# Kernel tuning notes

Measured on AMD Instinct MI355X. Metric: run time of the kernel, lower is better.

The kernel has to match this reference:

```python
import jax, jax.numpy as jnp
import numpy as np

B, KL, XL, DIM, H, PB = 4, 128, 4096, 256, 8, 8
HD = DIM // H
SCALE = HD ** -0.5
N_DIS = 64 + 2


def setup_inputs() -> dict:
    key = jax.random.key(0)
    ks = jax.random.split(key, 10)
    x = jax.random.normal(ks[0], (B, XL, DIM), jnp.float32)
    kernal = jax.random.normal(ks[1], (B, KL, DIM), jnp.float32)
    rd = jax.random.randint(ks[2], (B, KL, XL), 0, N_DIS)
    polar_pos = jax.random.randint(ks[3], (B, KL, XL), 0, PB)
    att_mask = jax.random.uniform(ks[4], (B, H, XL, KL)) < 0.1
    W_qkv = jax.random.normal(ks[5], (DIM, 3 * DIM), jnp.float32) * 0.02
    dis_embed = jax.random.normal(ks[6], (N_DIS, H), jnp.float32) * 0.02
    polar_emb = jax.random.normal(ks[7], (PB, 1), jnp.float32) * 0.02
    W_proj = jax.random.normal(ks[8], (DIM, DIM), jnp.float32) * 0.02
    b_proj = jnp.zeros((DIM,), jnp.float32)
    return dict(x=x, kernal=kernal, rd=rd, polar_pos=polar_pos, att_mask=att_mask,
                W_qkv=W_qkv, dis_embed=dis_embed, polar_emb=polar_emb,
                W_proj=W_proj, b_proj=b_proj)


def _heads(t, h):
    b, n, d = t.shape
    return t.reshape(b, n, h, d // h).transpose(0, 2, 1, 3)  # b h n hd


def reference(x, kernal, rd, polar_pos, att_mask, W_qkv, dis_embed, polar_emb, W_proj, b_proj):
    b, xl, dim = x.shape
    kl = kernal.shape[1]
    h = H
    scale = (dim // h) ** -0.5

    q, k, v = [_heads(t, h) for t in jnp.split(x @ W_qkv, 3, axis=-1)]        # b h xl hd
    k_q, k_k, k_v = [_heads(t, h) for t in jnp.split(kernal @ W_qkv, 3, axis=-1)]  # b h kl hd

    rd_e = dis_embed[rd].transpose(0, 3, 1, 2)  # (b,kl,xl,h) -> (b,h,kl,xl)

    # kernel -> x attention scores
    k_x_attn = jnp.einsum('bhkd,bhxd->bhkx', k_q, k) * scale  # b h kl xl

    # main orientation: one-hot-weighted |attn| reduced over x, argmax over polar bins
    pp = jnp.broadcast_to(polar_pos[:, None], (b, h, kl, xl))  # b h kl xl
    polar_hot = jax.nn.one_hot(pp, PB, dtype=k_x_attn.dtype)   # b h kl xl o
    ori_sum = jnp.einsum('bhkx,bhkxo->bhko', jnp.abs(k_x_attn), polar_hot)
    main_ori = jnp.argmax(ori_sum, axis=-1)                    # b h kl
    new_polar = pp - main_ori[..., None]
    new_polar = jnp.where(new_polar < 0, new_polar + PB, new_polar)
    polar_bias = polar_emb[new_polar, 0]                       # b h kl xl

    mask_k = att_mask.transpose(0, 1, 3, 2)                    # b h kl xl
    k_x_attn = jnp.where(mask_k, jnp.asarray(-1e6, k_x_attn.dtype), k_x_attn)
    attn_k = jax.nn.softmax(k_x_attn + rd_e + polar_bias, axis=-1)
    k_out = jnp.einsum('bhkx,bhxd->bhkd', attn_k, v)
    k_out = k_out.transpose(0, 2, 1, 3).reshape(b, kl, dim) @ W_proj + b_proj

    # x -> kernel attention scores
    x_k_attn = jnp.einsum('bhxd,bhkd->bhxk', q, k_k) * scale   # b h xl kl
    x_k_attn = jnp.where(att_mask, jnp.asarray(-1e9, x_k_attn.dtype), x_k_attn)
    x_k_attn = jax.nn.softmax(x_k_attn + rd_e.transpose(0, 1, 3, 2)
                              + polar_bias.transpose(0, 1, 3, 2), axis=-1)
    x_out = jnp.einsum('bhxk,bhkd->bhxd', x_k_attn, k_v)
    x_out = x_out.transpose(0, 2, 1, 3).reshape(b, xl, dim) @ W_proj + b_proj

    return (x_out, k_out)
```

## Files before the change

### kernel.cpp

```cpp
#include <hip/hip_runtime.h>
#include <hip/hip_bf16.h>

#define B_    4
#define KL_   128
#define XL_   4096
#define DIM_  256
#define H_    8
#define HD_   32
#define PB_   8
#define NDIS_ 66
#define TDIM_ 768
#define SCALE_ 0.17677669529663687f
#define NS_   4
#define XCH_  (XL_ / NS_)
#define NCH2_ 64
#define KC2_  16

typedef float v4f __attribute__((ext_vector_type(4)));
typedef short v8s __attribute__((ext_vector_type(8)));

__device__ __forceinline__ unsigned short f2bf(float f) {
    __hip_bfloat16 h = __float2bfloat16(f);
    return __builtin_bit_cast(unsigned short, h);
}
__device__ __forceinline__ float bf2f(unsigned short u) {
    return __bfloat162float(__builtin_bit_cast(__hip_bfloat16, u));
}
__device__ __forceinline__ void cvt_hilo(float v, unsigned short& hi, unsigned short& lo) {
    hi = f2bf(v);
    lo = f2bf(v - bf2f(hi));
}

__global__ __launch_bounds__(256) void pack_mask(const int* __restrict__ att_mask,
                                                 unsigned int* __restrict__ mbits) {
    size_t wid = (size_t)blockIdx.x * 256 + threadIdx.x;
    const int* src = &att_mask[wid * 32];
    unsigned bits = 0;
#pragma unroll
    for (int i = 0; i < 8; ++i) {
        int4 m4 = *(const int4*)&src[i * 4];
        bits |= (m4.x ? 1u : 0u) << (i * 4 + 0);
        bits |= (m4.y ? 1u : 0u) << (i * 4 + 1);
        bits |= (m4.z ? 1u : 0u) << (i * 4 + 2);
        bits |= (m4.w ? 1u : 0u) << (i * 4 + 3);
    }
    mbits[wid] = bits;
}

__global__ __launch_bounds__(256) void cvt_mat(const float* __restrict__ A,
                                               unsigned short* __restrict__ Ah,
                                               unsigned short* __restrict__ Al,
                                               size_t n4) {
    size_t i = ((size_t)blockIdx.x * 256 + threadIdx.x);
    if (i >= n4) return;
    float4 v = *(const float4*)&A[i * 4];
    ushort4 h, l;
    cvt_hilo(v.x, h.x, l.x);
    cvt_hilo(v.y, h.y, l.y);
    cvt_hilo(v.z, h.z, l.z);
    cvt_hilo(v.w, h.w, l.w);
    *(ushort4*)&Ah[i * 4] = h;
    *(ushort4*)&Al[i * 4] = l;
}

__global__ __launch_bounds__(256) void cvt_wT(const float* __restrict__ W,
                                              unsigned short* __restrict__ Wh,
                                              unsigned short* __restrict__ Wl,
                                              int K, int N) {
    int n = blockIdx.x, k = threadIdx.x;
    float v = W[(size_t)k * N + n];
    unsigned short h, l;
    cvt_hilo(v, h, l);
    Wh[(size_t)n * K + k] = h;
    Wl[(size_t)n * K + k] = l;
}

__global__ __launch_bounds__(256) void cvt_kq(const float* __restrict__ qkv_k,
                                              unsigned short* __restrict__ Kqh_g,
                                              unsigned short* __restrict__ Kql_g) {
    const int bh = blockIdx.x;
    const int b = bh >> 3, h = bh & 7;
    const int tid = threadIdx.x;
    const int k = tid >> 1, dg = (tid & 1) * 16;
    const float* src = &qkv_k[((size_t)(b * KL_ + k)) * TDIM_ + h * HD_ + dg];
    unsigned short hi[16], lo[16];
#pragma unroll
    for (int j4 = 0; j4 < 4; ++j4) {
        float4 v = *(const float4*)&src[j4 * 4];
        cvt_hilo(v.x, hi[j4 * 4 + 0], lo[j4 * 4 + 0]);
        cvt_hilo(v.y, hi[j4 * 4 + 1], lo[j4 * 4 + 1]);
        cvt_hilo(v.z, hi[j4 * 4 + 2], lo[j4 * 4 + 2]);
        cvt_hilo(v.w, hi[j4 * 4 + 3], lo[j4 * 4 + 3]);
    }
    unsigned short* dh = &Kqh_g[((size_t)bh * KL_ + k) * HD_ + dg];
    unsigned short* dl = &Kql_g[((size_t)bh * KL_ + k) * HD_ + dg];
    *(uint4*)&dh[0] = *(uint4*)&hi[0];
    *(uint4*)&dh[8] = *(uint4*)&hi[8];
    *(uint4*)&dl[0] = *(uint4*)&lo[0];
    *(uint4*)&dl[8] = *(uint4*)&lo[8];
}

__global__ __launch_bounds__(256) void gemm_mfma(const unsigned short* __restrict__ Ah,
                                                 const unsigned short* __restrict__ Al,
                                                 const unsigned short* __restrict__ Bh,
                                                 const unsigned short* __restrict__ Bl,
                                                 float* __restrict__ C,
                                                 const float* __restrict__ bias,
                                                 int M, int N, int K) {
    __shared__ __align__(16) unsigned short Ah_s[128][40];
    __shared__ __align__(16) unsigned short Al_s[128][40];
    __shared__ __align__(16) unsigned short Bh_s[128][40];
    __shared__ __align__(16) unsigned short Bl_s[128][40];
    const int tid = threadIdx.x;
    const int w = tid >> 6, lane = tid & 63;
    const int c = lane & 15, q = lane >> 4;
    const int bm = blockIdx.y * 128, bn = blockIdx.x * 128;
    const int srow = tid >> 1, shf = (tid & 1) * 16;

    v4f acc[2][8] = {};
    for (int k0 = 0; k0 < K; k0 += 32) {
        __syncthreads();
        {
            const size_t ab = (size_t)(bm + srow) * K + k0 + shf;
            *(uint4*)&Ah_s[srow][shf] = *(const uint4*)&Ah[ab];
            *(uint4*)&Ah_s[srow][shf + 8] = *(const uint4*)&Ah[ab + 8];
            *(uint4*)&Al_s[srow][shf] = *(const uint4*)&Al[ab];
            *(uint4*)&Al_s[srow][shf + 8] = *(const uint4*)&Al[ab + 8];
            const size_t bb = (size_t)(bn + srow) * K + k0 + shf;
            *(uint4*)&Bh_s[srow][shf] = *(const uint4*)&Bh[bb];
            *(uint4*)&Bh_s[srow][shf + 8] = *(const uint4*)&Bh[bb + 8];
            *(uint4*)&Bl_s[srow][shf] = *(const uint4*)&Bl[bb];
            *(uint4*)&Bl_s[srow][shf + 8] = *(const uint4*)&Bl[bb + 8];
        }
        __syncthreads();
        v8s afh[2], afl[2];
#pragma unroll
        for (int mt = 0; mt < 2; ++mt) {
            afh[mt] = *(v8s*)&Ah_s[w * 32 + mt * 16 + c][q * 8];
            afl[mt] = *(v8s*)&Al_s[w * 32 + mt * 16 + c][q * 8];
        }
#pragma unroll
        for (int nt = 0; nt < 8; ++nt) {
            v8s bfh = *(v8s*)&Bh_s[nt * 16 + c][q * 8];
            v8s bfl = *(v8s*)&Bl_s[nt * 16 + c][q * 8];
#pragma unroll
            for (int mt = 0; mt < 2; ++mt) {
                acc[mt][nt] = __builtin_amdgcn_mfma_f32_16x16x32_bf16(afl[mt], bfh, acc[mt][nt], 0, 0, 0);
                acc[mt][nt] = __builtin_amdgcn_mfma_f32_16x16x32_bf16(afh[mt], bfl, acc[mt][nt], 0, 0, 0);
                acc[mt][nt] = __builtin_amdgcn_mfma_f32_16x16x32_bf16(afh[mt], bfh, acc[mt][nt], 0, 0, 0);
            }
        }
    }
#pragma unroll
    for (int mt = 0; mt < 2; ++mt) {
#pragma unroll
        for (int nt = 0; nt < 8; ++nt) {
            int col = bn + nt * 16 + c;
            float bv = bias ? bias[col] : 0.0f;
#pragma unroll
            for (int r = 0; r < 4; ++r) {
                int row = bm + w * 32 + mt * 16 + q * 4 + r;
                C[(size_t)row * N + col] = acc[mt][nt][r] + bv;
            }
        }
    }
}

__global__ __launch_bounds__(256) void gemm64(const float* __restrict__ A,
                                              const float* __restrict__ Bw,
                                              float* __restrict__ C,
                                              const float* __restrict__ bias,
                                              int M, int N, int K) {
    __shared__ __align__(16) float As[16][68];
    __shared__ __align__(16) float Bs[16][64];
    const int tid = threadIdx.x;
    const int tx = tid & 15, ty = tid >> 4;
    const int bn = blockIdx.x * 64, bm = blockIdx.y * 64;
    const int am = tid >> 2, ac = tid & 3;
    float acc[4][4] = {};
    for (int k0 = 0; k0 < K; k0 += 16) {
        float4 a4 = *(const float4*)&A[(size_t)(bm + am) * K + k0 + ac * 4];
        As[ac * 4 + 0][am] = a4.x;
        As[ac * 4 + 1][am] = a4.y;
        As[ac * 4 + 2][am] = a4.z;
        As[ac * 4 + 3][am] = a4.w;
        *(float4*)&Bs[ty][tx * 4] = *(const float4*)&Bw[(size_t)(k0 + ty) * N + bn + tx * 4];
        __syncthreads();
#pragma unroll
        for (int kk = 0; kk < 16; ++kk) {
            float4 av = *(const float4*)&As[kk][ty * 4];
            float4 bv = *(const float4*)&Bs[kk][tx * 4];
            float a[4] = {av.x, av.y, av.z, av.w};
            float b[4] = {bv.x, bv.y, bv.z, bv.w};
#pragma unroll
            for (int i = 0; i < 4; ++i)
#pragma unroll
                for (int j = 0; j < 4; ++j) acc[i][j] += a[i] * b[j];
        }
        __syncthreads();
    }
#pragma unroll
    for (int i = 0; i < 4; ++i) {
        int m = bm + ty * 4 + i;
#pragma unroll
        for (int j = 0; j < 4; ++j) {
            int n = bn + tx * 4 + j;
            float v = acc[i][j];
            if (bias) v += bias[n];
            C[(size_t)m * N + n] = v;
        }
    }
}

__global__ __launch_bounds__(256) void score_bins_mfma4(const float* __restrict__ qkv_x,
                                                        const unsigned short* __restrict__ Kqh_g,
                                                        const unsigned short* __restrict__ Kql_g,
                                                        const int* __restrict__ rd,
                                                        const int* __restrict__ polar_pos,
                                                        const unsigned int* __restrict__ mbits,
                                                        const float* __restrict__ dis_embed,
                                                        __hip_bfloat16* __restrict__ Sg,
                                                        float* __restrict__ binspart) {
    const int b = blockIdx.z, h = blockIdx.y, xc = blockIdx.x;
    const int x0 = xc * 64;
    const int tid = threadIdx.x;
    const int w = tid >> 6, lane = tid & 63;
    const int c15 = lane & 15, q = lane >> 4;
    const size_t bh = (size_t)(b * H_ + h);

    __shared__ unsigned int mskb[64][5];
    __shared__ float de_h[NDIS_];
    __shared__ float binsL[8][4][16][PB_];
    __shared__ __align__(16) unsigned short Ss[2][16][72];

    {
        int xr = tid >> 2, kg = tid & 3;
        mskb[xr][kg] = mbits[(bh * XL_ + x0 + xr) * 4 + kg];
    }
    if (tid < NDIS_) de_h[tid] = dis_embed[tid * H_ + h];
    __syncthreads();

    v8s axh, axl;
    {
        const float* src = &qkv_x[((size_t)b * XL_ + x0 + w * 16 + c15) * TDIM_ + DIM_ + h * HD_ + q * 8];
        float4 v0 = *(const float4*)&src[0];
        float4 v1 = *(const float4*)&src[4];
        float vv[8] = {v0.x, v0.y, v0.z, v0.w, v1.x, v1.y, v1.z, v1.w};
#pragma unroll
        for (int j = 0; j < 8; ++j) {
            unsigned short hi, lo;
            cvt_hilo(vv[j], hi, lo);
            ((short*)&axh)[j] = (short)hi;
            ((short*)&axl)[j] = (short)lo;
        }
    }

    v8s bqh[2], bql[2];
    int4 r4[2], p4[2];
    auto load_nt = [&](int nt, int s) {
        const int k = nt * 16 + c15;
        const size_t kqoff = (bh * KL_ + k) * HD_ + q * 8;
        bqh[s] = *(const v8s*)&Kqh_g[kqoff];
        bql[s] = *(const v8s*)&Kql_g[kqoff];
        const size_t rowoff = ((size_t)(b * KL_ + k)) * XL_ + x0 + w * 16 + q * 4;
        r4[s] = *(const int4*)&rd[rowoff];
        p4[s] = *(const int4*)&polar_pos[rowoff];
    };
    load_nt(0, 0);

#pragma unroll
    for (int nt = 0; nt < 8; ++nt) {
        const int s = nt & 1;
        if (nt < 7) load_nt(nt + 1, s ^ 1);

        const int k = nt * 16 + c15;
        v4f D = {0.f, 0.f, 0.f, 0.f};
        D = __builtin_amdgcn_mfma_f32_16x16x32_bf16(axl, bqh[s], D, 0, 0, 0);
        D = __builtin_amdgcn_mfma_f32_16x16x32_bf16(axh, bql[s], D, 0, 0, 0);
        D = __builtin_amdgcn_mfma_f32_16x16x32_bf16(axh, bqh[s], D, 0, 0, 0);

        float bins[PB_] = {};
        {
            int rv[4] = {r4[s].x, r4[s].y, r4[s].z, r4[s].w};
            int pv[4] = {p4[s].x, p4[s].y, p4[s].z, p4[s].w};
            ushort4 pack;
#pragma unroll
            for (int r = 0; r < 4; ++r) {
                float sc = D[r] * SCALE_;
                float a = fabsf(sc);
                int pp = pv[r];
#pragma unroll
                for (int pb = 0; pb < PB_; ++pb) bins[pb] += (pp == pb) ? a : 0.0f;
                int xloc = w * 16 + q * 4 + r;
                int mbit = (mskb[xloc][k >> 5] >> (k & 31)) & 1;
                float sp = (mbit ? -1e6f : sc) + de_h[rv[r]];
                ((unsigned short*)&pack)[r] = f2bf(sp);
            }
            *(ushort4*)&Ss[s][c15][w * 16 + q * 4] = pack;
        }

#pragma unroll
        for (int pb = 0; pb < PB_; ++pb) {
            bins[pb] += __shfl_xor(bins[pb], 16);
            bins[pb] += __shfl_xor(bins[pb], 32);
        }
        if (q == 0) {
#pragma unroll
            for (int pb = 0; pb < PB_; ++pb) binsL[nt][w][c15][pb] = bins[pb];
        }

        __syncthreads();
        {
            int row = tid >> 4, seg = tid & 15;
            unsigned short* dst = (unsigned short*)Sg +
                (bh * KL_ + nt * 16 + row) * XL_ + x0 + seg * 4;
            *(uint2*)dst = *(const uint2*)&Ss[s][row][seg * 4];
        }
    }
    __syncthreads();
    {
        int k = tid >> 1, half = tid & 1;
        int nt = k >> 4, c = k & 15;
        float4 s = {0.f, 0.f, 0.f, 0.f};
#pragma unroll
        for (int w4 = 0; w4 < 4; ++w4) {
            float4 v = *(float4*)&binsL[nt][w4][c][half * 4];
            s.x += v.x; s.y += v.y; s.z += v.z; s.w += v.w;
        }
        *(float4*)&binspart[(bh * KL_ + k) * (NCH2_ * PB_) + xc * PB_ + half * 4] = s;
    }
}

__global__ __launch_bounds__(256) void bins_argmax(const float* __restrict__ binspart,
                                                   int* __restrict__ main_ori) {
    const int w = threadIdx.x >> 6, lane = threadIdx.x & 63;
    const int row = blockIdx.x * 4 + w;
    float s[PB_];
#pragma unroll
    for (int pb = 0; pb < PB_; ++pb) s[pb] = 0.0f;
    if (lane < NCH2_) {
        const float* bp = &binspart[(size_t)row * (NCH2_ * PB_) + lane * PB_];
#pragma unroll
        for (int pb = 0; pb < PB_; ++pb) s[pb] = bp[pb];
    }
#pragma unroll
    for (int m = 1; m < 64; m <<= 1)
#pragma unroll
        for (int pb = 0; pb < PB_; ++pb) s[pb] += __shfl_xor(s[pb], m);
    if (lane == 0) {
        float best = s[0];
        int bi = 0;
#pragma unroll
        for (int pb = 1; pb < PB_; ++pb)
            if (s[pb] > best) { best = s[pb]; bi = pb; }
        main_ori[row] = bi;
    }
}

__global__ __launch_bounds__(256) void flash_cached2(const float* __restrict__ qkv_x,
                                                     const __hip_bfloat16* __restrict__ Sg,
                                                     const int* __restrict__ polar_pos,
                                                     const float* __restrict__ polar_emb,
                                                     const int* __restrict__ main_ori,
                                                     float* __restrict__ part) {
    const int b = blockIdx.z, h = blockIdx.y;
    const int kch = blockIdx.x / NS_, xc = blockIdx.x % NS_;
    const int k0 = kch * KC2_;
    const int tid = threadIdx.x;
    const int ki = tid >> 4, xt = tid & 15;

    __shared__ __align__(16) float4 vs[64][9];
    __shared__ int pol_s[KC2_][68];
    __shared__ float pe[PB_];

    if (tid < PB_) pe[tid] = polar_emb[tid];
    const size_t xbase = (size_t)b * XL_;
    const size_t bh = (size_t)(b * H_ + h);
    const size_t row_k = bh * KL_ + k0 + ki;
    const int mo = main_ori[row_k];
    const int xbeg = xc * XCH_;

    float l = 0.f;
    float4 acc[8] = {};
    __syncthreads();
    for (int t = 0; t < XCH_ / 64; ++t) {
        const int x0 = xbeg + t * 64;
        __syncthreads();
#pragma unroll
        for (int i = 0; i < 2; ++i) {
            int id = tid + 256 * i;
            int row = id >> 3, c = id & 7;
            vs[row][c] = *(const float4*)&qkv_x[(xbase + x0 + row) * TDIM_ + 2 * DIM_ + h * HD_ + c * 4];
        }
        {
            int kk = tid >> 4, c = tid & 15;
            *(int4*)&pol_s[kk][c * 4] =
                *(const int4*)&polar_pos[(size_t)(b * KL_ + k0 + kk) * XL_ + x0 + c * 4];
        }
        __syncthreads();
#pragma unroll
        for (int j = 0; j < 4; ++j) {
            int xl = xt + 16 * j;
            int x = x0 + xl;
            float sp = __bfloat162float(Sg[row_k * XL_ + x]);
            int pp = pol_s[ki][xl];
            int np = pp - mo;
            np += (np >> 31) & PB_;
            float p = __expf(sp + pe[np]);
            l += p;
#pragma unroll
            for (int c = 0; c < 8; ++c) {
                float4 v = vs[xl][c];
                acc[c].x += p * v.x; acc[c].y += p * v.y;
                acc[c].z += p * v.z; acc[c].w += p * v.w;
            }
        }
    }
#pragma unroll
    for (int m = 1; m < 16; m <<= 1) {
        l += __shfl_xor(l, m, 16);
#pragma unroll
        for (int c = 0; c < 8; ++c) {
            acc[c].x += __shfl_xor(acc[c].x, m, 16);
            acc[c].y += __shfl_xor(acc[c].y, m, 16);
            acc[c].z += __shfl_xor(acc[c].z, m, 16);
            acc[c].w += __shfl_xor(acc[c].w, m, 16);
        }
    }
    if (xt == 0) {
        float* dst = &part[(size_t)(row_k * NS_ + xc) * 36];
#pragma unroll
        for (int c = 0; c < 8; ++c) *(float4*)&dst[c * 4] = acc[c];
        dst[32] = l;
    }
}

__global__ __launch_bounds__(256) void merge_cached(const float* __restrict__ part,
                                                    float* __restrict__ kout_pre) {
    const int tid = threadIdx.x;
    const int ri = tid >> 5, d = tid & 31;
    const int row = blockIdx.x * 8 + ri;
    float l = 0.f, a = 0.f;
#pragma unroll
    for (int c = 0; c < NS_; ++c) {
        const float* p = &part[(size_t)(row * NS_ + c) * 36];
        l += p[32];
        a += p[d];
    }
    int k = row & (KL_ - 1);
    int bh = row >> 7;
    int h = bh & (H_ - 1), b = bh >> 3;
    kout_pre[(size_t)(b * KL_ + k) * DIM_ + h * HD_ + d] = a / l;
}

__global__ __launch_bounds__(256) void attn_x_mfma(const float* __restrict__ qkv_x,
                                                   const float* __restrict__ qkv_k,
                                                   const int* __restrict__ rd,
                                                   const int* __restrict__ polar_pos,
                                                   const unsigned int* __restrict__ mbits,
                                                   const float* __restrict__ dis_embed,
                                                   const float* __restrict__ polar_emb,
                                                   const int* __restrict__ main_ori,
                                                   unsigned short* __restrict__ oh,
                                                   unsigned short* __restrict__ ol) {
    const int b = blockIdx.z, h = blockIdx.y;
    const int x0 = blockIdx.x * 64;
    const int tid = threadIdx.x;
    const int wave = tid >> 6, lane = tid & 63;
    const int c = lane & 15, q = lane >> 4;

    __shared__ __align__(16) unsigned short Kk_s[KL_][40];
    __shared__ __align__(16) unsigned short VT_s[HD_][136];
    __shared__ __align__(16) unsigned short P_s[4][16][136];
    __shared__ unsigned short rp_s[KL_][72];
    __shared__ unsigned int msk_s[64][5];
    __shared__ float de_h[NDIS_];
    __shared__ float pe[PB_];
    __shared__ int mo_s[KL_];

    const size_t bh = (size_t)(b * H_ + h);
    if (tid < NDIS_) de_h[tid] = dis_embed[tid * H_ + h];
    if (tid < PB_) pe[tid] = polar_emb[tid];
    if (tid < KL_) mo_s[tid] = main_ori[bh * KL_ + tid];

    {
        int row = tid >> 1, half = tid & 1;
        const float* src = &qkv_k[(size_t)(b * KL_ + row) * TDIM_ + h * HD_ + half * 16];
#pragma unroll
        for (int j = 0; j < 16; ++j) Kk_s[row][half * 16 + j] = f2bf(src[DIM_ + j]);
#pragma unroll
        for (int j = 0; j < 16; ++j) VT_s[half * 16 + j][row] = f2bf(src[2 * DIM_ + j]);
    }
    {
        int xr = tid >> 2, kg = tid & 3;
        msk_s[xr][kg] = mbits[(bh * XL_ + x0 + xr) * 4 + kg];
    }
    __syncthreads();

#pragma unroll
    for (int i = 0; i < 8; ++i) {
        int id = tid + 256 * i;
        int k = id >> 4, cc = id & 15;
        size_t gb = (size_t)(b * KL_ + k) * XL_ + x0 + cc * 4;
        int4 r4 = *(const int4*)&rd[gb];
        int4 p4 = *(const int4*)&polar_pos[gb];
        int mo = mo_s[k];
        int n0 = p4.x - mo; n0 += (n0 >> 31) & PB_;
        int n1 = p4.y - mo; n1 += (n1 >> 31) & PB_;
        int n2 = p4.z - mo; n2 += (n2 >> 31) & PB_;
        int n3 = p4.w - mo; n3 += (n3 >> 31) & PB_;
        rp_s[k][cc * 4 + 0] = (unsigned short)(r4.x | (n0 << 8));
        rp_s[k][cc * 4 + 1] = (unsigned short)(r4.y | (n1 << 8));
        rp_s[k][cc * 4 + 2] = (unsigned short)(r4.z | (n2 << 8));
        rp_s[k][cc * 4 + 3] = (unsigned short)(r4.w | (n3 << 8));
    }
    __syncthreads();

    v8s aq;
    {
        const float* qp = &qkv_x[(size_t)(b * XL_ + x0 + wave * 16 + c) * TDIM_ + h * HD_ + q * 8];
        float4 q0 = *(const float4*)&qp[0];
        float4 q1 = *(const float4*)&qp[4];
        aq[0] = (short)f2bf(q0.x); aq[1] = (short)f2bf(q0.y);
        aq[2] = (short)f2bf(q0.z); aq[3] = (short)f2bf(q0.w);
        aq[4] = (short)f2bf(q1.x); aq[5] = (short)f2bf(q1.y);
        aq[6] = (short)f2bf(q1.z); aq[7] = (short)f2bf(q1.w);
    }

    v4f S[8];
#pragma unroll
    for (int t = 0; t < 8; ++t) {
        v8s bk = *(v8s*)&Kk_s[t * 16 + c][q * 8];
        S[t] = __builtin_amdgcn_mfma_f32_16x16x32_bf16(aq, bk, (v4f){0.f, 0.f, 0.f, 0.f}, 0, 0, 0);
    }

    const int xloc = wave * 16;
    float lr[4] = {0.f, 0.f, 0.f, 0.f};
#pragma unroll
    for (int t = 0; t < 8; ++t) {
#pragma unroll
        for (int r = 0; r < 4; ++r) {
            int krow = t * 16 + c;
            int xrow = q * 4 + r;
            unsigned short rp = rp_s[krow][xloc + xrow];
            int mbit = (msk_s[xloc + xrow][krow >> 5] >> (krow & 31)) & 1;
            float sval = S[t][r] * SCALE_;
            float tval = (mbit ? -25.0f : sval) + de_h[rp & 0x7f] + pe[(rp >> 8) & 7];
            float p = __expf(tval);
            unsigned short pb = f2bf(p);
            P_s[wave][xrow][krow] = pb;
            lr[r] += bf2f(pb);
        }
    }
#pragma unroll
    for (int r = 0; r < 4; ++r) {
#pragma unroll
        for (int m = 1; m < 16; m <<= 1) lr[r] += __shfl_xor(lr[r], m);
    }
    __syncthreads();

    v4f O0 = {0.f, 0.f, 0.f, 0.f}, O1 = {0.f, 0.f, 0.f, 0.f};
#pragma unroll
    for (int kc = 0; kc < 4; ++kc) {
        v8s ap = *(v8s*)&P_s[wave][c][kc * 32 + q * 8];
        v8s bv0 = *(v8s*)&VT_s[c][kc * 32 + q * 8];
        v8s bv1 = *(v8s*)&VT_s[16 + c][kc * 32 + q * 8];
        O0 = __builtin_amdgcn_mfma_f32_16x16x32_bf16(ap, bv0, O0, 0, 0, 0);
        O1 = __builtin_amdgcn_mfma_f32_16x16x32_bf16(ap, bv1, O1, 0, 0, 0);
    }

#pragma unroll
    for (int r = 0; r < 4; ++r) {
        int xg = x0 + wave * 16 + q * 4 + r;
        float inv = 1.0f / lr[r];
        size_t obase = (size_t)(b * XL_ + xg) * DIM_ + h * HD_;
        float v0 = O0[r] * inv;
        float v1 = O1[r] * inv;
        unsigned short h0, l0, h1, l1;
        cvt_hilo(v0, h0, l0);
        cvt_hilo(v1, h1, l1);
        oh[obase + c] = h0;
        ol[obase + c] = l0;
        oh[obase + 16 + c] = h1;
        ol[obase + 16 + c] = l1;
    }
}

extern "C" void kernel_launch(void* const* d_in, const int* in_sizes, int n_in,
                              void* d_out, int out_size, void* d_ws, size_t ws_size,
                              hipStream_t stream) {
    const float* x         = (const float*)d_in[0];
    const float* kernal    = (const float*)d_in[1];
    const int* rd          = (const int*)d_in[2];
    const int* polar_pos   = (const int*)d_in[3];
    const int* att_mask    = (const int*)d_in[4];
    const float* W_qkv     = (const float*)d_in[5];
    const float* dis_embed = (const float*)d_in[6];
    const float* polar_emb = (const float*)d_in[7];
    const float* W_proj    = (const float*)d_in[8];
    const float* b_proj    = (const float*)d_in[9];
    float* out             = (float*)d_out;

    char* base = (char*)d_ws;
    size_t off = 0;
    auto alloc = [&](size_t bytes) { void* p = base + off; off = (off + bytes + 255) & ~255ULL; return p; };
    float* qkv_x    = (float*)alloc((size_t)B_ * XL_ * TDIM_ * 4);
    float* qkv_k    = (float*)alloc((size_t)B_ * KL_ * TDIM_ * 4);
    float* xout_pre = (float*)alloc((size_t)B_ * XL_ * DIM_ * 4);
    float* kout_pre = (float*)alloc((size_t)B_ * KL_ * DIM_ * 4);
    int* main_ori   = (int*)alloc(B_ * H_ * KL_ * 4);
    float* part     = (float*)alloc((size_t)B_ * H_ * KL_ * NS_ * 36 * 4);
    __hip_bfloat16* Sg = (__hip_bfloat16*)alloc((size_t)B_ * H_ * KL_ * XL_ * 2);
    unsigned short* wph = (unsigned short*)alloc((size_t)DIM_ * DIM_ * 2);
    unsigned short* wpl = (unsigned short*)alloc((size_t)DIM_ * DIM_ * 2);
    unsigned int* mbits = (unsigned int*)alloc((size_t)B_ * H_ * XL_ * (KL_ / 32) * 4);

    float* binspart = xout_pre;
    const size_t MX = (size_t)B_ * XL_;
    unsigned short* xh = (unsigned short*)Sg;
    unsigned short* xl_ = xh + MX * DIM_;
    unsigned short* wqh = (unsigned short*)part;
    unsigned short* wql = wqh + (size_t)TDIM_ * DIM_;
    unsigned short* kqh_g = wqh + 2 * (size_t)TDIM_ * DIM_;
    unsigned short* kql_g = kqh_g + (size_t)B_ * H_ * KL_ * HD_;
    unsigned short* oh = (unsigned short*)Sg;
    unsigned short* ol = oh + MX * DIM_;

    pack_mask<<<dim3((B_ * H_ * XL_ * (KL_ / 32)) / 256), 256, 0, stream>>>(att_mask, mbits);
    cvt_mat<<<dim3((MX * DIM_ / 4 + 255) / 256), 256, 0, stream>>>(x, xh, xl_, MX * DIM_ / 4);
    cvt_wT<<<dim3(TDIM_), DIM_, 0, stream>>>(W_qkv, wqh, wql, DIM_, TDIM_);
    cvt_wT<<<dim3(DIM_), DIM_, 0, stream>>>(W_proj, wph, wpl, DIM_, DIM_);

    gemm_mfma<<<dim3(TDIM_ / 128, MX / 128), 256, 0, stream>>>(
        xh, xl_, wqh, wql, qkv_x, nullptr, MX, TDIM_, DIM_);
    gemm64<<<dim3(TDIM_ / 64, (B_ * KL_) / 64), 256, 0, stream>>>(
        kernal, W_qkv, qkv_k, nullptr, B_ * KL_, TDIM_, DIM_);
    cvt_kq<<<dim3(B_ * H_), 256, 0, stream>>>(qkv_k, kqh_g, kql_g);

    score_bins_mfma4<<<dim3(NCH2_, H_, B_), 256, 0, stream>>>(
        qkv_x, kqh_g, kql_g, rd, polar_pos, mbits, dis_embed, Sg, binspart);
    bins_argmax<<<dim3(B_ * H_ * KL_ / 4), 256, 0, stream>>>(binspart, main_ori);
    flash_cached2<<<dim3((KL_ / KC2_) * NS_, H_, B_), 256, 0, stream>>>(
        qkv_x, Sg, polar_pos, polar_emb, main_ori, part);
    merge_cached<<<dim3(B_ * H_ * KL_ / 8), 256, 0, stream>>>(part, kout_pre);

    attn_x_mfma<<<dim3(XL_ / 64, H_, B_), 256, 0, stream>>>(
        qkv_x, qkv_k, rd, polar_pos, mbits, dis_embed, polar_emb, main_ori, oh, ol);

    gemm_mfma<<<dim3(DIM_ / 128, MX / 128), 256, 0, stream>>>(
        oh, ol, wph, wpl, out, b_proj, MX, DIM_, DIM_);
    gemm64<<<dim3(DIM_ / 64, (B_ * KL_) / 64), 256, 0, stream>>>(
        kout_pre, W_proj, out + (size_t)B_ * XL_ * DIM_, b_proj, B_ * KL_, DIM_, DIM_);
}
```

Measured before the change: 350.4 us.

## Use direct global-to-LDS loads in GEMM and write scores straight to global

The GEMM tile loads now use global_load_lds to move bf16 hi/lo tiles directly into unpadded LDS, bypassing registers, with an explicit vmcnt wait before the barrier. The score kernel drops its LDS staging buffer and per-iteration barrier, writing each packed 4-element bf16 vector directly to global memory. The first removes register round-trips but loses the LDS padding, which may cause bank conflicts on fragment reads. The second removes a sync but issues narrower, less coalesced global stores.

```diff
diff --git a/kernel.cpp b/kernel.cpp
--- a/kernel.cpp
+++ b/kernel.cpp
@@ -107,42 +107,53 @@
                                                  float* __restrict__ C,
                                                  const float* __restrict__ bias,
                                                  int M, int N, int K) {
-    __shared__ __align__(16) unsigned short Ah_s[128][40];
-    __shared__ __align__(16) unsigned short Al_s[128][40];
-    __shared__ __align__(16) unsigned short Bh_s[128][40];
-    __shared__ __align__(16) unsigned short Bl_s[128][40];
+    __shared__ __align__(16) unsigned short Ah_s[128 * 32];
+    __shared__ __align__(16) unsigned short Al_s[128 * 32];
+    __shared__ __align__(16) unsigned short Bh_s[128 * 32];
+    __shared__ __align__(16) unsigned short Bl_s[128 * 32];
     const int tid = threadIdx.x;
     const int w = tid >> 6, lane = tid & 63;
     const int c = lane & 15, q = lane >> 4;
     const int bm = blockIdx.y * 128, bn = blockIdx.x * 128;
-    const int srow = tid >> 1, shf = (tid & 1) * 16;
+
+    const int lrow = lane >> 2;
+    const int lcol = (lane & 3) * 8;
 
     v4f acc[2][8] = {};
     for (int k0 = 0; k0 < K; k0 += 32) {
         __syncthreads();
-        {
-            const size_t ab = (size_t)(bm + srow) * K + k0 + shf;
-            *(uint4*)&Ah_s[srow][shf] = *(const uint4*)&Ah[ab];
-            *(uint4*)&Ah_s[srow][shf + 8] = *(const uint4*)&Ah[ab + 8];
-            *(uint4*)&Al_s[srow][shf] = *(const uint4*)&Al[ab];
-            *(uint4*)&Al_s[srow][shf + 8] = *(const uint4*)&Al[ab + 8];
-            const size_t bb = (size_t)(bn + srow) * K + k0 + shf;
-            *(uint4*)&Bh_s[srow][shf] = *(const uint4*)&Bh[bb];
-            *(uint4*)&Bh_s[srow][shf + 8] = *(const uint4*)&Bh[bb + 8];
-            *(uint4*)&Bl_s[srow][shf] = *(const uint4*)&Bl[bb];
-            *(uint4*)&Bl_s[srow][shf + 8] = *(const uint4*)&Bl[bb + 8];
-        }
+#pragma unroll
+        for (int i = 0; i < 2; ++i) {
+            const int chunk = w * 2 + i;
+            const int row = chunk * 16 + lrow;
+            const size_t ga = (size_t)(bm + row) * K + k0 + lcol;
+            const size_t gb = (size_t)(bn + row) * K + k0 + lcol;
+            const int lo = chunk * 512;
+            __builtin_amdgcn_global_load_lds(
+                (const __attribute__((address_space(1))) unsigned int*)&Ah[ga],
+                (__attribute__((address_space(3))) unsigned int*)&Ah_s[lo], 16, 0, 0);
+            __builtin_amdgcn_global_load_lds(
+                (const __attribute__((address_space(1))) unsigned int*)&Al[ga],
+                (__attribute__((address_space(3))) unsigned int*)&Al_s[lo], 16, 0, 0);
+            __builtin_amdgcn_global_load_lds(
+                (const __attribute__((address_space(1))) unsigned int*)&Bh[gb],
+                (__attribute__((address_space(3))) unsigned int*)&Bh_s[lo], 16, 0, 0);
+            __builtin_amdgcn_global_load_lds(
+                (const __attribute__((address_space(1))) unsigned int*)&Bl[gb],
+                (__attribute__((address_space(3))) unsigned int*)&Bl_s[lo], 16, 0, 0);
+        }
+        asm volatile("s_waitcnt vmcnt(0)" ::: "memory");
         __syncthreads();
         v8s afh[2], afl[2];
 #pragma unroll
         for (int mt = 0; mt < 2; ++mt) {
-            afh[mt] = *(v8s*)&Ah_s[w * 32 + mt * 16 + c][q * 8];
-            afl[mt] = *(v8s*)&Al_s[w * 32 + mt * 16 + c][q * 8];
+            afh[mt] = *(v8s*)&Ah_s[(w * 32 + mt * 16 + c) * 32 + q * 8];
+            afl[mt] = *(v8s*)&Al_s[(w * 32 + mt * 16 + c) * 32 + q * 8];
         }
 #pragma unroll
         for (int nt = 0; nt < 8; ++nt) {
-            v8s bfh = *(v8s*)&Bh_s[nt * 16 + c][q * 8];
-            v8s bfl = *(v8s*)&Bl_s[nt * 16 + c][q * 8];
+            v8s bfh = *(v8s*)&Bh_s[(nt * 16 + c) * 32 + q * 8];
+            v8s bfl = *(v8s*)&Bl_s[(nt * 16 + c) * 32 + q * 8];
 #pragma unroll
             for (int mt = 0; mt < 2; ++mt) {
                 acc[mt][nt] = __builtin_amdgcn_mfma_f32_16x16x32_bf16(afl[mt], bfh, acc[mt][nt], 0, 0, 0);
@@ -231,7 +242,6 @@
     __shared__ unsigned int mskb[64][5];
     __shared__ float de_h[NDIS_];
     __shared__ float binsL[8][4][16][PB_];
-    __shared__ __align__(16) unsigned short Ss[2][16][72];
 
     {
         int xr = tid >> 2, kg = tid & 3;
@@ -296,7 +306,7 @@
                 float sp = (mbit ? -1e6f : sc) + de_h[rv[r]];
                 ((unsigned short*)&pack)[r] = f2bf(sp);
             }
-            *(ushort4*)&Ss[s][c15][w * 16 + q * 4] = pack;
+            *(ushort4*)((unsigned short*)Sg + (bh * KL_ + k) * XL_ + x0 + w * 16 + q * 4) = pack;
         }
 
 #pragma unroll
@@ -307,14 +317,6 @@
         if (q == 0) {
 #pragma unroll
             for (int pb = 0; pb < PB_; ++pb) binsL[nt][w][c15][pb] = bins[pb];
-        }
-
-        __syncthreads();
-        {
-            int row = tid >> 4, seg = tid & 15;
-            unsigned short* dst = (unsigned short*)Sg +
-                (bh * KL_ + nt * 16 + row) * XL_ + x0 + seg * 4;
-            *(uint2*)dst = *(const uint2*)&Ss[s][row][seg * 4];
         }
     }
     __syncthreads();
```

Result: no change. 352.7 us (+0.7%).
